# Performance work log

Hardware: AMD Instinct MI355X
Metric: run time of the kernel (lower is better)

Reference implementation:

```python
import jax, jax.numpy as jnp
import numpy as np

B, C, N = 4, 256, 4096
OUT = 256
TEMP = OUT ** 0.5  # temperature = sqrt(out_channel)


def setup_inputs() -> dict:
    key = jax.random.key(0)
    kx, kxx, kq, kk, kv = jax.random.split(key, 5)
    x = jax.random.normal(kx, (B, C, N), dtype=jnp.float32)
    xx = jax.random.normal(kxx, (B, C, N), dtype=jnp.float32)
    # Conv1d(in, out, kernel=1, bias=False) weights, squeezed to (out, in)
    s = 1.0 / np.sqrt(C)
    Wq = jax.random.uniform(kq, (OUT, C), jnp.float32, -s, s)
    Wk = jax.random.uniform(kk, (OUT, C), jnp.float32, -s, s)
    Wv = jax.random.uniform(kv, (OUT, C), jnp.float32, -s, s)
    return {"x": x, "xx": xx, "Wq": Wq, "Wk": Wk, "Wv": Wv}


def reference(x, xx, Wq, Wk, Wv):
    # 1x1 conv == per-point linear: (out,in) x (b,in,n) -> (b,out,n)
    q = jnp.einsum('oc,bcn->bon', Wq, x)
    k = jnp.einsum('oc,bcn->bon', Wk, xx)
    v = jnp.einsum('oc,bcn->bon', Wv, xx)
    # attn = (q^T / temp) @ k : (B, N, N)
    attn = jax.nn.softmax(jnp.einsum('bon,bom->bnm', q, k) / TEMP, axis=-1)
    # dropout is identity in eval mode
    # y = attn @ v^T -> (B, N, OUT); returned transposed to (B, OUT, N)
    y = jnp.einsum('bnm,bom->bon', attn, v)
    return y
```

## Files before the change

### kernel.cpp

```cpp
#include <hip/hip_runtime.h>
#include <hip/hip_bf16.h>


typedef __attribute__((ext_vector_type(8))) short bf16x8;
typedef __attribute__((ext_vector_type(4))) float f32x4;
typedef __attribute__((ext_vector_type(4))) short short4t;

constexpr int B_ = 4;
constexpr int C_ = 256;
constexpr int N_ = 4096;
constexpr int O_ = 256;
constexpr float INV_TEMP = 1.0f / 16.0f;
constexpr int NIT = 64;

__device__ __forceinline__ short f2bf(float f) {
  union { float f; unsigned u; } v; v.f = f;
  unsigned r = v.u + 0x7fffu + ((v.u >> 16) & 1u);
  return (short)(r >> 16);
}

__global__ void wcvt(const float* __restrict__ Wq, const float* __restrict__ Wk,
                     const float* __restrict__ Wv, short* __restrict__ wb) {
  int i = blockIdx.x * 256 + threadIdx.x;
  int mat = i >> 16, off = i & 65535;
  const float* W = (mat == 0) ? Wq : (mat == 1 ? Wk : Wv);
  wb[i] = f2bf(W[off]);
}

__global__ __launch_bounds__(256, 2) void qkv_proj(
    const float* __restrict__ x, const float* __restrict__ xx,
    const short* __restrict__ wb,
    short* __restrict__ qg, short* __restrict__ kt, short* __restrict__ vt) {
  const int n0  = blockIdx.x * 64;
  const int b   = blockIdx.y;
  const int mat = blockIdx.z;
  const float* src = (mat == 0) ? x : xx;
  const short* W   = wb + mat * 65536;
  const int tid = threadIdx.x;
  const int w = tid >> 6, lane = tid & 63;
  const int g = lane >> 4, c16 = lane & 15;

  __shared__ __align__(16) short xs[64][264];

  {
    const int n = tid & 63, cq = tid >> 6;
    const float* sp = src + (size_t)b * C_ * N_ + n0 + n;
#pragma unroll
    for (int rep = 0; rep < 16; ++rep) {
      int c = rep * 16 + cq * 4;
      short4t s4;
#pragma unroll
      for (int j = 0; j < 4; ++j) s4[j] = f2bf(sp[(size_t)(c + j) * N_]);
      *(short4t*)&xs[n][c] = s4;
    }
  }
  __syncthreads();

  f32x4 acc[4][4];
#pragma unroll
  for (int i = 0; i < 4; ++i)
#pragma unroll
    for (int j = 0; j < 4; ++j) acc[i][j] = (f32x4){0.f, 0.f, 0.f, 0.f};

#pragma unroll
  for (int ko = 0; ko < 8; ++ko) {
    bf16x8 wfr[4], xfr[4];
#pragma unroll
    for (int ot = 0; ot < 4; ++ot)
      wfr[ot] = *(const bf16x8*)&W[(w * 64 + ot * 16 + c16) * C_ + ko * 32 + g * 8];
#pragma unroll
    for (int nt = 0; nt < 4; ++nt)
      xfr[nt] = *(const bf16x8*)&xs[nt * 16 + c16][ko * 32 + g * 8];
    if (mat < 2) {
#pragma unroll
      for (int ot = 0; ot < 4; ++ot)
#pragma unroll
        for (int nt = 0; nt < 4; ++nt)
          acc[ot][nt] = __builtin_amdgcn_mfma_f32_16x16x32_bf16(
              wfr[ot], xfr[nt], acc[ot][nt], 0, 0, 0);
    } else {
#pragma unroll
      for (int mt = 0; mt < 4; ++mt)
#pragma unroll
        for (int ot = 0; ot < 4; ++ot)
          acc[mt][ot] = __builtin_amdgcn_mfma_f32_16x16x32_bf16(
              xfr[mt], wfr[ot], acc[mt][ot], 0, 0, 0);
    }
  }

  __syncthreads();
  short* ob = &xs[0][0];

  if (mat == 0) {
#pragma unroll
    for (int ot = 0; ot < 4; ++ot)
#pragma unroll
      for (int nt = 0; nt < 4; ++nt) {
        int f = (nt * 16 + c16) * 256 + w * 64 + ot * 16 + g * 4;
        short4t s;
        s[0] = f2bf(acc[ot][nt][0] * INV_TEMP);
        s[1] = f2bf(acc[ot][nt][1] * INV_TEMP);
        s[2] = f2bf(acc[ot][nt][2] * INV_TEMP);
        s[3] = f2bf(acc[ot][nt][3] * INV_TEMP);
        *(short4t*)&ob[f] = s;
      }
  } else if (mat == 1) {
#pragma unroll
    for (int ot = 0; ot < 4; ++ot)
#pragma unroll
      for (int nt = 0; nt < 4; ++nt) {
        int koo = w * 2 + (ot >> 1);
        int pos = (((ot & 1) * 2 + (g >> 1)) ^ ((c16 >> 1) & 3));
        int f = nt * 4096 + koo * 512 + c16 * 32 + pos * 8 + (g & 1) * 4;
        short4t s;
        s[0] = f2bf(acc[ot][nt][0]);
        s[1] = f2bf(acc[ot][nt][1]);
        s[2] = f2bf(acc[ot][nt][2]);
        s[3] = f2bf(acc[ot][nt][3]);
        *(short4t*)&ob[f] = s;
      }
  } else {
#pragma unroll
    for (int mt = 0; mt < 4; ++mt)
#pragma unroll
      for (int ot = 0; ot < 4; ++ot) {
        int o = w * 64 + ot * 16 + c16;
        int pos = (mt * 2 + (g >> 1)) ^ (o & 7);
        int f = o * 64 + pos * 8 + (g & 1) * 4;
        short4t s;
        s[0] = f2bf(acc[mt][ot][0]);
        s[1] = f2bf(acc[mt][ot][1]);
        s[2] = f2bf(acc[mt][ot][2]);
        s[3] = f2bf(acc[mt][ot][3]);
        *(short4t*)&ob[f] = s;
      }
  }
  __syncthreads();

  short* dst = (mat == 0) ? qg + ((size_t)b * N_ + n0) * O_
             : (mat == 1) ? kt + (size_t)(b * 256 + (n0 >> 4)) * 4096
                          : vt + (size_t)(b * 64 + (n0 >> 6)) * 16384;
  const uint4* s4 = (const uint4*)ob;
  uint4* d4 = (uint4*)dst;
#pragma unroll
  for (int j = 0; j < 8; ++j) d4[j * 256 + tid] = s4[j * 256 + tid];
}

__global__ __launch_bounds__(512, 4) void flash_attn(
    const short* __restrict__ qg, const short* __restrict__ kt,
    const short* __restrict__ vt, float* __restrict__ out) {
  const int xg = blockIdx.x;
  const int b  = xg & 3;
  const int n0 = (((xg >> 2) << 5) + blockIdx.y) * 32;
  const int tid = threadIdx.x;
  const int w = tid >> 6, lane = tid & 63;
  const int g = lane >> 4, c16 = lane & 15;
  const int pw = w & 3;

  __shared__ short ps[2][32][72];
  __shared__ float lsum[4][32];

  const short* ktb = kt + (size_t)b * N_ * O_;
  const short* vtb = vt + (size_t)b * N_ * O_;

  if (w < 4) {
    bf16x8 qf[2][8];
    bf16x8 kf[8];
    float lrun[2] = {0.f, 0.f};
    const int koff = c16 * 32 + ((g ^ ((c16 >> 1) & 3)) * 8);

#pragma unroll
    for (int nt = 0; nt < 2; ++nt) {
      const short* qrow =
          qg + (size_t)(b * N_ + n0 + nt * 16 + c16) * O_ + g * 8;
#pragma unroll
      for (int ko = 0; ko < 8; ++ko)
        qf[nt][ko] = *(const bf16x8*)(qrow + ko * 32);
    }
    {
      const short* kg = ktb + (size_t)pw * 4096;
#pragma unroll
      for (int j = 0; j < 8; ++j)
        kf[j] = *(const bf16x8*)(kg + j * 512 + koff);
    }

    for (int i = 0; i <= NIT; ++i) {
      if (i < NIT) {
        f32x4 sacc[2];
#pragma unroll
        for (int nt = 0; nt < 2; ++nt) sacc[nt] = (f32x4){0.f, 0.f, 0.f, 0.f};
        __builtin_amdgcn_s_setprio(1);
#pragma unroll
        for (int ko = 0; ko < 8; ++ko) {
#pragma unroll
          for (int nt = 0; nt < 2; ++nt)
            sacc[nt] = __builtin_amdgcn_mfma_f32_16x16x32_bf16(
                kf[ko], qf[nt][ko], sacc[nt], 0, 0, 0);
        }
        __builtin_amdgcn_s_setprio(0);
        if (i + 1 < NIT) {
          const short* kg = ktb + (size_t)(4 * (i + 1) + pw) * 4096;
#pragma unroll
          for (int j = 0; j < 8; ++j)
            kf[j] = *(const bf16x8*)(kg + j * 512 + koff);
        }
#pragma unroll
        for (int nt = 0; nt < 2; ++nt) {
          short4t pb;
          float rs = 0.f;
#pragma unroll
          for (int r = 0; r < 4; ++r) {
            float p = __expf(sacc[nt][r]);
            rs += p;
            pb[r] = f2bf(p);
          }
          lrun[nt] += rs;
          *(short4t*)&ps[i & 1][nt * 16 + c16][pw * 16 + g * 4] = pb;
        }
      }
      asm volatile("s_waitcnt lgkmcnt(0)" ::: "memory");
      __builtin_amdgcn_s_barrier();
    }
#pragma unroll
    for (int nt = 0; nt < 2; ++nt) {
      float v = lrun[nt];
      v += __shfl_xor(v, 16);
      v += __shfl_xor(v, 32);
      if (lane < 16) lsum[pw][nt * 16 + lane] = v;
    }
    asm volatile("s_waitcnt lgkmcnt(0)" ::: "memory");
    __builtin_amdgcn_s_barrier();
  } else {
    bf16x8 vf[8];
    f32x4 oacc[4][2];
#pragma unroll
    for (int i = 0; i < 4; ++i)
#pragma unroll
      for (int j = 0; j < 2; ++j) oacc[i][j] = (f32x4){0.f, 0.f, 0.f, 0.f};

    for (int i = 0; i <= NIT; ++i) {
      if (i > 0) {
        const int pb_ = (i - 1) & 1;
        __builtin_amdgcn_s_setprio(1);
#pragma unroll
        for (int kk = 0; kk < 2; ++kk) {
          bf16x8 pf[2];
#pragma unroll
          for (int nt = 0; nt < 2; ++nt)
            pf[nt] = *(const bf16x8*)&ps[pb_][nt * 16 + c16][kk * 32 + g * 8];
#pragma unroll
          for (int ot = 0; ot < 4; ++ot) {
#pragma unroll
            for (int nt = 0; nt < 2; ++nt)
              oacc[ot][nt] = __builtin_amdgcn_mfma_f32_16x16x32_bf16(
                  vf[kk * 4 + ot], pf[nt], oacc[ot][nt], 0, 0, 0);
          }
        }
        __builtin_amdgcn_s_setprio(0);
      }
      if (i < NIT) {
        const short* vg = vtb + (size_t)i * 16384;
#pragma unroll
        for (int kk = 0; kk < 2; ++kk)
#pragma unroll
          for (int ot = 0; ot < 4; ++ot)
            vf[kk * 4 + ot] = *(const bf16x8*)(
                vg + (pw * 64 + ot * 16 + c16) * 64 +
                ((kk * 4 + g) ^ (c16 & 7)) * 8);
      }
      asm volatile("s_waitcnt lgkmcnt(0)" ::: "memory");
      __builtin_amdgcn_s_barrier();
    }
    __builtin_amdgcn_s_barrier();

#pragma unroll
    for (int nt = 0; nt < 2; ++nt) {
      const int nl = nt * 16 + c16;
      float l = lsum[0][nl] + lsum[1][nl] + lsum[2][nl] + lsum[3][nl];
      float li = 1.0f / l;
#pragma unroll
      for (int ot = 0; ot < 4; ++ot) {
        float* op = out + ((size_t)b * O_ + pw * 64 + ot * 16 + g * 4) * N_ +
                    n0 + nl;
#pragma unroll
        for (int r = 0; r < 4; ++r)
          op[(size_t)r * N_] = oacc[ot][nt][r] * li;
      }
    }
  }
}

extern "C" void kernel_launch(void* const* d_in, const int* in_sizes, int n_in,
                              void* d_out, int out_size, void* d_ws,
                              size_t ws_size, hipStream_t stream) {
  const float* x  = (const float*)d_in[0];
  const float* xx = (const float*)d_in[1];
  const float* Wq = (const float*)d_in[2];
  const float* Wk = (const float*)d_in[3];
  const float* Wv = (const float*)d_in[4];
  float* out = (float*)d_out;

  short* qg = (short*)d_ws;
  short* kt = qg + (size_t)B_ * N_ * O_;
  short* vt = kt + (size_t)B_ * N_ * O_;
  short* wb = vt + (size_t)B_ * N_ * O_;

  wcvt<<<768, 256, 0, stream>>>(Wq, Wk, Wv, wb);
  qkv_proj<<<dim3(N_ / 64, B_, 3), 256, 0, stream>>>(x, xx, wb, qg, kt, vt);
  flash_attn<<<dim3(16, 32), 512, 0, stream>>>(qg, kt, vt, out);
}
```

Measured before the change: 190.9 us.

## Share xx tile between K and V projections and vectorize input loads

The projection kernel now launches two z-slices instead of three: one computes Q from x, the other loads the xx tile once and computes K and V in two sequential passes, removing a redundant global read and conversion of xx. The input staging switches from scalar strided float loads to 16-byte vector loads, followed by an in-register transpose into shared memory with rotated column order to spread bank conflicts. A separate shared output buffer is added so the input tile survives across passes, which raises LDS use per block and may lower occupancy. The K/V blocks also do twice the work, so the load across blocks is uneven.

```diff
diff --git a/kernel.cpp b/kernel.cpp
--- a/kernel.cpp
+++ b/kernel.cpp
@@ -31,119 +31,133 @@
     const float* __restrict__ x, const float* __restrict__ xx,
     const short* __restrict__ wb,
     short* __restrict__ qg, short* __restrict__ kt, short* __restrict__ vt) {
-  const int n0  = blockIdx.x * 64;
-  const int b   = blockIdx.y;
-  const int mat = blockIdx.z;
-  const float* src = (mat == 0) ? x : xx;
-  const short* W   = wb + mat * 65536;
+  const int n0 = blockIdx.x * 64;
+  const int b  = blockIdx.y;
+  const int kv = blockIdx.z;
+  const float* src = kv ? xx : x;
   const int tid = threadIdx.x;
   const int w = tid >> 6, lane = tid & 63;
   const int g = lane >> 4, c16 = lane & 15;
 
   __shared__ __align__(16) short xs[64][264];
+  __shared__ __align__(16) short ob[16384];
 
   {
-    const int n = tid & 63, cq = tid >> 6;
-    const float* sp = src + (size_t)b * C_ * N_ + n0 + n;
-#pragma unroll
-    for (int rep = 0; rep < 16; ++rep) {
-      int c = rep * 16 + cq * 4;
-      short4t s4;
-#pragma unroll
-      for (int j = 0; j < 4; ++j) s4[j] = f2bf(sp[(size_t)(c + j) * N_]);
-      *(short4t*)&xs[n][c] = s4;
-    }
+    const int q  = tid & 15;
+    const int rg = tid >> 4;
+    const float* sp = src + (size_t)b * C_ * N_ + n0 + q * 4;
+    f32x4 v[16];
+#pragma unroll
+    for (int i = 0; i < 16; ++i)
+      v[i] = *(const f32x4*)(sp + (size_t)(rg * 16 + i) * N_);
+#pragma unroll
+    for (int jj = 0; jj < 4; ++jj)
+#pragma unroll
+      for (int k = 0; k < 4; ++k) {
+        const int i4 = (k + q) & 3;
+        short4t s4;
+#pragma unroll
+        for (int j = 0; j < 4; ++j) s4[j] = f2bf(v[i4 * 4 + j][jj]);
+        *(short4t*)&xs[q * 4 + jj][rg * 16 + i4 * 4] = s4;
+      }
   }
   __syncthreads();
 
-  f32x4 acc[4][4];
-#pragma unroll
-  for (int i = 0; i < 4; ++i)
-#pragma unroll
-    for (int j = 0; j < 4; ++j) acc[i][j] = (f32x4){0.f, 0.f, 0.f, 0.f};
-
-#pragma unroll
-  for (int ko = 0; ko < 8; ++ko) {
-    bf16x8 wfr[4], xfr[4];
-#pragma unroll
-    for (int ot = 0; ot < 4; ++ot)
-      wfr[ot] = *(const bf16x8*)&W[(w * 64 + ot * 16 + c16) * C_ + ko * 32 + g * 8];
-#pragma unroll
-    for (int nt = 0; nt < 4; ++nt)
-      xfr[nt] = *(const bf16x8*)&xs[nt * 16 + c16][ko * 32 + g * 8];
-    if (mat < 2) {
+  const int npass = kv ? 2 : 1;
+#pragma unroll 1
+  for (int p = 0; p < npass; ++p) {
+    const int mat = kv ? (1 + p) : 0;
+    const short* W = wb + mat * 65536;
+
+    f32x4 acc[4][4];
+#pragma unroll
+    for (int i = 0; i < 4; ++i)
+#pragma unroll
+      for (int j = 0; j < 4; ++j) acc[i][j] = (f32x4){0.f, 0.f, 0.f, 0.f};
+
+#pragma unroll
+    for (int ko = 0; ko < 8; ++ko) {
+      bf16x8 wfr[4], xfr[4];
 #pragma unroll
       for (int ot = 0; ot < 4; ++ot)
-#pragma unroll
-        for (int nt = 0; nt < 4; ++nt)
-          acc[ot][nt] = __builtin_amdgcn_mfma_f32_16x16x32_bf16(
-              wfr[ot], xfr[nt], acc[ot][nt], 0, 0, 0);
+        wfr[ot] = *(const bf16x8*)&W[(w * 64 + ot * 16 + c16) * C_ +
+                                     ko * 32 + g * 8];
+#pragma unroll
+      for (int nt = 0; nt < 4; ++nt)
+        xfr[nt] = *(const bf16x8*)&xs[nt * 16 + c16][ko * 32 + g * 8];
+      if (mat < 2) {
+#pragma unroll
+        for (int ot = 0; ot < 4; ++ot)
+#pragma unroll
+          for (int nt = 0; nt < 4; ++nt)
+            acc[ot][nt] = __builtin_amdgcn_mfma_f32_16x16x32_bf16(
+                wfr[ot], xfr[nt], acc[ot][nt], 0, 0, 0);
+      } else {
+#pragma unroll
+        for (int mt = 0; mt < 4; ++mt)
+#pragma unroll
+          for (int ot = 0; ot < 4; ++ot)
+            acc[mt][ot] = __builtin_amdgcn_mfma_f32_16x16x32_bf16(
+                xfr[mt], wfr[ot], acc[mt][ot], 0, 0, 0);
+      }
+    }
+
+    if (mat == 0) {
+#pragma unroll
+      for (int ot = 0; ot < 4; ++ot)
+#pragma unroll
+        for (int nt = 0; nt < 4; ++nt) {
+          int f = (nt * 16 + c16) * 256 + w * 64 + ot * 16 + g * 4;
+          short4t s;
+          s[0] = f2bf(acc[ot][nt][0] * INV_TEMP);
+          s[1] = f2bf(acc[ot][nt][1] * INV_TEMP);
+          s[2] = f2bf(acc[ot][nt][2] * INV_TEMP);
+          s[3] = f2bf(acc[ot][nt][3] * INV_TEMP);
+          *(short4t*)&ob[f] = s;
+        }
+    } else if (mat == 1) {
+#pragma unroll
+      for (int ot = 0; ot < 4; ++ot)
+#pragma unroll
+        for (int nt = 0; nt < 4; ++nt) {
+          int koo = w * 2 + (ot >> 1);
+          int pos = (((ot & 1) * 2 + (g >> 1)) ^ ((c16 >> 1) & 3));
+          int f = nt * 4096 + koo * 512 + c16 * 32 + pos * 8 + (g & 1) * 4;
+          short4t s;
+          s[0] = f2bf(acc[ot][nt][0]);
+          s[1] = f2bf(acc[ot][nt][1]);
+          s[2] = f2bf(acc[ot][nt][2]);
+          s[3] = f2bf(acc[ot][nt][3]);
+          *(short4t*)&ob[f] = s;
+        }
     } else {
 #pragma unroll
       for (int mt = 0; mt < 4; ++mt)
 #pragma unroll
-        for (int ot = 0; ot < 4; ++ot)
-          acc[mt][ot] = __builtin_amdgcn_mfma_f32_16x16x32_bf16(
-              xfr[mt], wfr[ot], acc[mt][ot], 0, 0, 0);
-    }
+        for (int ot = 0; ot < 4; ++ot) {
+          int o = w * 64 + ot * 16 + c16;
+          int pos = (mt * 2 + (g >> 1)) ^ (o & 7);
+          int f = o * 64 + pos * 8 + (g & 1) * 4;
+          short4t s;
+          s[0] = f2bf(acc[mt][ot][0]);
+          s[1] = f2bf(acc[mt][ot][1]);
+          s[2] = f2bf(acc[mt][ot][2]);
+          s[3] = f2bf(acc[mt][ot][3]);
+          *(short4t*)&ob[f] = s;
+        }
+    }
+    __syncthreads();
+
+    short* dst = (mat == 0) ? qg + ((size_t)b * N_ + n0) * O_
+               : (mat == 1) ? kt + (size_t)(b * 256 + (n0 >> 4)) * 4096
+                            : vt + (size_t)(b * 64 + (n0 >> 6)) * 16384;
+    const uint4* s4p = (const uint4*)ob;
+    uint4* d4 = (uint4*)dst;
+#pragma unroll
+    for (int j = 0; j < 8; ++j) d4[j * 256 + tid] = s4p[j * 256 + tid];
+
+    if (p + 1 < npass) __syncthreads();
   }
-
-  __syncthreads();
-  short* ob = &xs[0][0];
-
-  if (mat == 0) {
-#pragma unroll
-    for (int ot = 0; ot < 4; ++ot)
-#pragma unroll
-      for (int nt = 0; nt < 4; ++nt) {
-        int f = (nt * 16 + c16) * 256 + w * 64 + ot * 16 + g * 4;
-        short4t s;
-        s[0] = f2bf(acc[ot][nt][0] * INV_TEMP);
-        s[1] = f2bf(acc[ot][nt][1] * INV_TEMP);
-        s[2] = f2bf(acc[ot][nt][2] * INV_TEMP);
-        s[3] = f2bf(acc[ot][nt][3] * INV_TEMP);
-        *(short4t*)&ob[f] = s;
-      }
-  } else if (mat == 1) {
-#pragma unroll
-    for (int ot = 0; ot < 4; ++ot)
-#pragma unroll
-      for (int nt = 0; nt < 4; ++nt) {
-        int koo = w * 2 + (ot >> 1);
-        int pos = (((ot & 1) * 2 + (g >> 1)) ^ ((c16 >> 1) & 3));
-        int f = nt * 4096 + koo * 512 + c16 * 32 + pos * 8 + (g & 1) * 4;
-        short4t s;
-        s[0] = f2bf(acc[ot][nt][0]);
-        s[1] = f2bf(acc[ot][nt][1]);
-        s[2] = f2bf(acc[ot][nt][2]);
-        s[3] = f2bf(acc[ot][nt][3]);
-        *(short4t*)&ob[f] = s;
-      }
-  } else {
-#pragma unroll
-    for (int mt = 0; mt < 4; ++mt)
-#pragma unroll
-      for (int ot = 0; ot < 4; ++ot) {
-        int o = w * 64 + ot * 16 + c16;
-        int pos = (mt * 2 + (g >> 1)) ^ (o & 7);
-        int f = o * 64 + pos * 8 + (g & 1) * 4;
-        short4t s;
-        s[0] = f2bf(acc[mt][ot][0]);
-        s[1] = f2bf(acc[mt][ot][1]);
-        s[2] = f2bf(acc[mt][ot][2]);
-        s[3] = f2bf(acc[mt][ot][3]);
-        *(short4t*)&ob[f] = s;
-      }
-  }
-  __syncthreads();
-
-  short* dst = (mat == 0) ? qg + ((size_t)b * N_ + n0) * O_
-             : (mat == 1) ? kt + (size_t)(b * 256 + (n0 >> 4)) * 4096
-                          : vt + (size_t)(b * 64 + (n0 >> 6)) * 16384;
-  const uint4* s4 = (const uint4*)ob;
-  uint4* d4 = (uint4*)dst;
-#pragma unroll
-  for (int j = 0; j < 8; ++j) d4[j * 256 + tid] = s4[j * 256 + tid];
 }
 
 __global__ __launch_bounds__(512, 4) void flash_attn(
@@ -306,6 +320,6 @@
   short* wb = vt + (size_t)B_ * N_ * O_;
 
   wcvt<<<768, 256, 0, stream>>>(Wq, Wk, Wv, wb);
-  qkv_proj<<<dim3(N_ / 64, B_, 3), 256, 0, stream>>>(x, xx, wb, qg, kt, vt);
+  qkv_proj<<<dim3(N_ / 64, B_, 2), 256, 0, stream>>>(x, xx, wb, qg, kt, vt);
   flash_attn<<<dim3(16, 32), 512, 0, stream>>>(qg, kt, vt, out);
 }
```

Measured after the change: 200.8 us. 5.2% more time.
